# Performance work log

Hardware: AMD Instinct MI355X
Metric: run time of the kernel (lower is better)

Reference implementation:

```python
import jax, jax.numpy as jnp
import numpy as np

B, S, D, H = 256, 512, 128, 256  # batch, seq_len, input_dim, hidden_dim


def setup_inputs() -> dict:
    key = jax.random.key(0)
    ks = jax.random.split(key, 7)
    scale = 1.0 / np.sqrt(H)
    return {
        "x": jax.random.normal(ks[0], (B, S, D), dtype=jnp.float32),
        # WU_e: Linear(2H + S -> S, bias=False)
        "W_ue": jax.random.uniform(ks[1], (S, 2 * H + S), dtype=jnp.float32, minval=-scale, maxval=scale),
        # v_e: Linear(S -> 1, bias=False)
        "v_e": jax.random.uniform(ks[2], (1, S), dtype=jnp.float32, minval=-scale, maxval=scale),
        # LSTM params (PyTorch layout: gates order i,f,g,o)
        "W_ih": jax.random.uniform(ks[3], (4 * H, D), dtype=jnp.float32, minval=-scale, maxval=scale),
        "W_hh": jax.random.uniform(ks[4], (4 * H, H), dtype=jnp.float32, minval=-scale, maxval=scale),
        "b_ih": jax.random.uniform(ks[5], (4 * H,), dtype=jnp.float32, minval=-scale, maxval=scale),
        "b_hh": jax.random.uniform(ks[6], (4 * H,), dtype=jnp.float32, minval=-scale, maxval=scale),
    }


def reference(x, W_ue, v_e, W_ih, W_hh, b_ih, b_hh):
    b = x.shape[0]
    hdim = W_hh.shape[1]
    # Split WU_e into the part acting on (h,c) and the part acting on x rows.
    W_h = W_ue[:, : 2 * hdim]          # [S, 2H]
    W_x = W_ue[:, 2 * hdim:]           # [S, S]
    xT = jnp.transpose(x, (0, 2, 1))   # [B, D, S]
    # x contribution to attention logits is the same every step -> precompute.
    proj_x = jnp.einsum("bds,os->bdo", xT, W_x)  # [B, D, S]
    v = v_e[0]                          # [S]
    xs = jnp.transpose(x, (1, 0, 2))    # [S, B, D]

    def step(carry, x_t):
        h, c = carry                                    # [B, H] each
        hs = jnp.concatenate([h, c], axis=-1)           # [B, 2H]
        proj_h = hs @ W_h.T                             # [B, S]
        t = jnp.tanh(proj_h[:, None, :] + proj_x)       # [B, D, S]
        E = jnp.einsum("bds,s->bd", t, v)               # [B, D]
        alpha = jax.nn.softmax(E, axis=1)               # [B, D]
        inp = x_t * alpha                               # [B, D]
        gates = inp @ W_ih.T + b_ih + h @ W_hh.T + b_hh # [B, 4H]
        i, f, g, o = jnp.split(gates, 4, axis=-1)
        i = jax.nn.sigmoid(i)
        f = jax.nn.sigmoid(f)
        g = jnp.tanh(g)
        o = jax.nn.sigmoid(o)
        c_new = f * c + i * g
        h_new = o * jnp.tanh(c_new)
        return (h_new, c_new), h_new

    h0 = jnp.zeros((b, hdim), dtype=x.dtype)
    c0 = jnp.zeros((b, hdim), dtype=x.dtype)
    _, x_encoded = jax.lax.scan(step, (h0, c0), xs)  # [S, B, H]
    return x_encoded
```

## Files before the change

### kernel.cpp

```cpp
#include <hip/hip_runtime.h>
#include <hip/hip_bf16.h>

typedef __attribute__((ext_vector_type(8))) short bf16x8;
typedef __attribute__((ext_vector_type(4))) float f32x4;

#define C2LE 2.8853900817779268f
#define LOG2E 1.4426950408889634f
#define AGENT __HIP_MEMORY_SCOPE_AGENT
#define RLX __ATOMIC_RELAXED

static __device__ __forceinline__ float blo(unsigned q) { return __uint_as_float(q << 16); }
static __device__ __forceinline__ float bhi(unsigned q) { return __uint_as_float(q & 0xFFFF0000u); }
static __device__ __forceinline__ float rterm(float arg) {
  return __builtin_amdgcn_rcpf(1.0f + __builtin_amdgcn_exp2f(arg));
}
static __device__ __forceinline__ float sigm(float x) {
  return __builtin_amdgcn_rcpf(1.0f + __builtin_amdgcn_exp2f(-x * LOG2E));
}
static __device__ __forceinline__ float tanhe(float x) {
  return fmaf(-2.0f, __builtin_amdgcn_rcpf(1.0f + __builtin_amdgcn_exp2f(x * C2LE)), 1.0f);
}
static __device__ __forceinline__ unsigned packhilo(float x) {
  __hip_bfloat16 h = __float2bfloat16(x);
  float r = x - __bfloat162float(h);
  __hip_bfloat16 l = __float2bfloat16(r);
  return (unsigned)__bfloat16_as_ushort(h) | ((unsigned)__bfloat16_as_ushort(l) << 16);
}
static __device__ __forceinline__ void mkfrags(uint4 q0, uint4 q1, bf16x8& hi, bf16x8& lo) {
  uint4 h, l;
  h.x = __builtin_amdgcn_perm(q0.y, q0.x, 0x05040100u);
  h.y = __builtin_amdgcn_perm(q0.w, q0.z, 0x05040100u);
  h.z = __builtin_amdgcn_perm(q1.y, q1.x, 0x05040100u);
  h.w = __builtin_amdgcn_perm(q1.w, q1.z, 0x05040100u);
  l.x = __builtin_amdgcn_perm(q0.y, q0.x, 0x07060302u);
  l.y = __builtin_amdgcn_perm(q0.w, q0.z, 0x07060302u);
  l.z = __builtin_amdgcn_perm(q1.y, q1.x, 0x07060302u);
  l.w = __builtin_amdgcn_perm(q1.w, q1.z, 0x07060302u);
  hi = *(bf16x8*)&h;
  lo = *(bf16x8*)&l;
}

__global__ void k_pack_whB(const float* __restrict__ wue, __hip_bfloat16* __restrict__ wp) {
  for (int idx = blockIdx.x * blockDim.x + threadIdx.x; idx < 262144;
       idx += gridDim.x * blockDim.x) {
    int j = idx & 7, l = (idx >> 3) & 63, kap = (idx >> 9) & 15, nb = (idx >> 13) & 3,
        sl = idx >> 15;
    int o = sl * 64 + nb * 16 + (l & 15);
    int dim = kap * 32 + (l >> 4) * 8 + j;
    wp[idx] = __float2bfloat16(wue[o * 1024 + dim]);
  }
}
__global__ void k_pack_w3B(const float* __restrict__ wih, const float* __restrict__ whh,
                           __hip_bfloat16* __restrict__ wp) {
  for (int idx = blockIdx.x * blockDim.x + threadIdx.x; idx < 393216;
       idx += gridDim.x * blockDim.x) {
    int j = idx & 7, l = (idx >> 3) & 63;
    int ks = (idx >> 9) % 12, r = (idx >> 9) / 12;
    int nb = r & 7, sl = r >> 3;
    int n = nb * 16 + (l & 15);
    int g = (n >> 5) * 256 + sl * 32 + (n & 31);
    int k = ks * 32 + (l >> 4) * 8 + j;
    float v = (k < 128) ? wih[g * 128 + k] : whh[g * 256 + (k - 128)];
    wp[idx] = __float2bfloat16(v);
  }
}
__global__ void k_bsum(const float* __restrict__ bih, const float* __restrict__ bhh,
                       float* __restrict__ bs) {
  int idx = blockIdx.x * blockDim.x + threadIdx.x;
  if (idx < 1024) bs[idx] = bih[idx] + bhh[idx];
}
__global__ void k_wxt(const float* __restrict__ wue, float* __restrict__ wxt) {
  for (int idx = blockIdx.x * blockDim.x + threadIdx.x; idx < 512 * 512;
       idx += gridDim.x * blockDim.x) {
    int o = idx & 511, s = idx >> 9;
    wxt[idx] = wue[o * 1024 + 512 + s];
  }
}

__global__ __launch_bounds__(512) void k_projx(const float* __restrict__ x,
                                               const float* __restrict__ wxt,
                                               __hip_bfloat16* __restrict__ px2) {
  __shared__ alignas(16) float xsT[32][512];
  const int b = blockIdx.x;
  const int tid = threadIdx.x;
  for (int dt = 0; dt < 4; ++dt) {
    __syncthreads();
    const float4* xr = (const float4*)(x + ((size_t)b << 16) + (size_t)tid * 128 + dt * 32);
#pragma unroll
    for (int q = 0; q < 8; ++q) {
      float4 vx = xr[q];
      xsT[q * 4 + 0][tid] = vx.x;
      xsT[q * 4 + 1][tid] = vx.y;
      xsT[q * 4 + 2][tid] = vx.z;
      xsT[q * 4 + 3][tid] = vx.w;
    }
    __syncthreads();
    const int o = tid;
    float acc[32];
#pragma unroll
    for (int dd = 0; dd < 32; ++dd) acc[dd] = 0.f;
    for (int s4 = 0; s4 < 128; ++s4) {
      float w0 = wxt[(s4 * 4 + 0) * 512 + o];
      float w1 = wxt[(s4 * 4 + 1) * 512 + o];
      float w2 = wxt[(s4 * 4 + 2) * 512 + o];
      float w3 = wxt[(s4 * 4 + 3) * 512 + o];
#pragma unroll
      for (int dd = 0; dd < 32; ++dd) {
        float4 xv = *(const float4*)&xsT[dd][s4 * 4];
        acc[dd] = fmaf(w0, xv.x, fmaf(w1, xv.y, fmaf(w2, xv.z, fmaf(w3, xv.w, acc[dd]))));
      }
    }
    for (int dd = 0; dd < 32; ++dd) {
      px2[((size_t)b * 128 + dt * 32 + dd) * 512 + o] = __float2bfloat16(acc[dd] * C2LE);
    }
  }
}

static __device__ __forceinline__ void gbar(unsigned* ctr, unsigned target) {
  __syncthreads();
  if (threadIdx.x == 0) {
    __hip_atomic_fetch_add(ctr, 1u, RLX, AGENT);
    while (__hip_atomic_load(ctr, RLX, AGENT) < target) __builtin_amdgcn_s_sleep(1);
  }
  __syncthreads();
}

__global__ __launch_bounds__(1024) void k_main(
    const __hip_bfloat16* __restrict__ px2, const __hip_bfloat16* __restrict__ whB,
    const __hip_bfloat16* __restrict__ w3B, const float* __restrict__ bsum,
    const float* __restrict__ x, const float* __restrict__ ve,
    unsigned* __restrict__ hG, float* __restrict__ Eg, unsigned* __restrict__ ctrs,
    float* __restrict__ out) {
  __shared__ alignas(16) __hip_bfloat16 w3_l[49152];
  __shared__ alignas(16) unsigned hA[8192];
  __shared__ alignas(16) unsigned uA[2048];
  __shared__ float PHp[4][8][64];
  __shared__ float PH[512];
  __shared__ float gp[2][128][8];
  __shared__ float c_l[32][8];
  __shared__ float v_l[64];
  __shared__ float bs_l[128];
  __shared__ float zpart[16];
  __shared__ float vss_sh;

  const int grp = blockIdx.x & 31;
  const int sl = blockIdx.x >> 5;
  const int tid = threadIdx.x;
  const int lane = tid & 63;
  const int w = tid >> 6;
  const int b = tid >> 7;
  const int d = tid & 127;
  const int bG = grp * 8 + b;

  {
    const uint4* src = (const uint4*)(w3B + (size_t)sl * 49152);
    uint4* dst = (uint4*)w3_l;
    for (int i = tid; i < 6144; i += 1024) dst[i] = src[i];
  }
  bf16x8 whr[4];
  {
    const bf16x8* src =
        (const bf16x8*)whB + ((size_t)(sl * 4 + (w & 3)) * 16 + (w >> 2) * 4) * 64 + lane;
#pragma unroll
    for (int i = 0; i < 4; ++i) whr[i] = src[i * 64];
  }
  uint4 pxr[8];
  {
    const uint4* p4 = (const uint4*)(px2 + ((size_t)bG * 128 + d) * 512 + sl * 64);
#pragma unroll
    for (int i = 0; i < 8; ++i) pxr[i] = p4[i];
  }
  if (tid < 64) v_l[tid] = ve[sl * 64 + tid];
  if (tid < 128) bs_l[tid] = bsum[(tid >> 5) * 256 + sl * 32 + (tid & 31)];
  if (tid < 256) c_l[tid >> 3][tid & 7] = 0.f;
  for (int i = tid; i < 8192; i += 1024) hA[i] = 0;
  for (int i = tid; i < 2048; i += 1024) uA[i] = 0;
  if (tid == 0) {
    float s = 0.f;
    for (int i = 0; i < 64; ++i) s += ve[sl * 64 + i];
    vss_sh = s;
  }
  __syncthreads();
  const float vss = vss_sh;
  unsigned* ctrA = ctrs + grp * 64;
  unsigned* ctrB = ctrA + 32;

  for (int t = 0; t < 512; ++t) {
    const int par = t & 1;

    {
      const unsigned long long* hp =
          (const unsigned long long*)(hG + (size_t)(par * 32 + grp) * 4096) + tid * 2;
      unsigned long long a0 = __hip_atomic_load(hp, RLX, AGENT);
      unsigned long long a1 = __hip_atomic_load(hp + 1, RLX, AGENT);
      int p = tid * 4;
      int jb = p & 7, bb = (p >> 3) & 7, rest = p >> 6;
      uint4 q;
      q.x = (unsigned)a0;
      q.y = (unsigned)(a0 >> 32);
      q.z = (unsigned)a1;
      q.w = (unsigned)(a1 >> 32);
      *(uint4*)&hA[rest * 128 + bb * 8 + jb] = q;
    }
    if (tid < 128)
      __hip_atomic_store(Eg + (size_t)((1 - par) * 32 + grp) * 1024 + sl * 128 + tid, 0.f, RLX,
                         AGENT);
    __syncthreads();

    {
      const int kq = w >> 2, nb = w & 3;
      f32x4 acc = {0.f, 0.f, 0.f, 0.f};
#pragma unroll
      for (int i = 0; i < 4; ++i) {
        const uint4* ap = (const uint4*)&hA[((kq * 4 + i) * 64 + lane) * 8];
        uint4 q0 = ap[0], q1 = ap[1];
        bf16x8 ahi, alo;
        mkfrags(q0, q1, ahi, alo);
        acc = __builtin_amdgcn_mfma_f32_16x16x32_bf16(ahi, whr[i], acc, 0, 0, 0);
        acc = __builtin_amdgcn_mfma_f32_16x16x32_bf16(alo, whr[i], acc, 0, 0, 0);
      }
      if (lane < 32) {
        int r16 = lane >> 4, c16 = lane & 15;
#pragma unroll
        for (int rr = 0; rr < 4; ++rr) PHp[kq][r16 * 4 + rr][nb * 16 + c16] = acc[rr];
      }
    }
    __syncthreads();
    if (tid < 512)
      PH[tid] = (PHp[0][tid >> 6][tid & 63] + PHp[1][tid >> 6][tid & 63] +
                 PHp[2][tid >> 6][tid & 63] + PHp[3][tid >> 6][tid & 63]) *
                C2LE;
    __syncthreads();

    float xv = x[((size_t)bG * 512 + t) * 128 + d];
    {
      float R = 0.f;
      const float* PHb = &PH[b * 64];
#pragma unroll 2
      for (int s8 = 0; s8 < 8; ++s8) {
        uint4 q = pxr[s8];
        float4 pa = *(const float4*)&PHb[s8 * 8];
        float4 pb = *(const float4*)&PHb[s8 * 8 + 4];
        float4 va = *(const float4*)&v_l[s8 * 8];
        float4 vb = *(const float4*)&v_l[s8 * 8 + 4];
        R = fmaf(va.x, rterm(pa.x + blo(q.x)), R);
        R = fmaf(va.y, rterm(pa.y + bhi(q.x)), R);
        R = fmaf(va.z, rterm(pa.z + blo(q.y)), R);
        R = fmaf(va.w, rterm(pa.w + bhi(q.y)), R);
        R = fmaf(vb.x, rterm(pb.x + blo(q.z)), R);
        R = fmaf(vb.y, rterm(pb.y + bhi(q.z)), R);
        R = fmaf(vb.z, rterm(pb.z + blo(q.w)), R);
        R = fmaf(vb.w, rterm(pb.w + bhi(q.w)), R);
      }
      __hip_atomic_fetch_add(Eg + (size_t)(par * 32 + grp) * 1024 + b * 128 + d,
                             fmaf(-2.f, R, vss), RLX, AGENT);
    }
    gbar(ctrA, 8u * (t + 1));

    float Ev = __hip_atomic_load(Eg + (size_t)(par * 32 + grp) * 1024 + b * 128 + d, RLX, AGENT);
    float e = __builtin_amdgcn_exp2f(Ev * LOG2E);
    {
      float z = e;
#pragma unroll
      for (int m = 1; m < 64; m <<= 1) z += __shfl_xor(z, m);
      if (lane == 0) zpart[w] = z;
    }
    __syncthreads();
    {
      float zf = zpart[2 * b] + zpart[2 * b + 1];
      float u = xv * e * __builtin_amdgcn_rcpf(zf);
      uA[((d >> 5) * 64 + ((d >> 3) & 3) * 16 + b) * 8 + (d & 7)] = packhilo(u);
    }
    __syncthreads();

    {
      const int nb = w & 7, kh = w >> 3;
      f32x4 acc = {0.f, 0.f, 0.f, 0.f};
      const bf16x8* bp = (const bf16x8*)w3_l + ((size_t)nb * 12 + kh * 6) * 64 + lane;
#pragma unroll
      for (int i = 0; i < 6; ++i) {
        int ks = kh * 6 + i;
        const uint4* ap = (ks < 4) ? (const uint4*)&uA[(ks * 64 + lane) * 8]
                                   : (const uint4*)&hA[((ks - 4) * 64 + lane) * 8];
        uint4 q0 = ap[0], q1 = ap[1];
        bf16x8 ahi, alo;
        mkfrags(q0, q1, ahi, alo);
        bf16x8 bf = bp[i * 64];
        acc = __builtin_amdgcn_mfma_f32_16x16x32_bf16(ahi, bf, acc, 0, 0, 0);
        acc = __builtin_amdgcn_mfma_f32_16x16x32_bf16(alo, bf, acc, 0, 0, 0);
      }
      if (lane < 32) {
        int r16 = lane >> 4, c16 = lane & 15;
#pragma unroll
        for (int rr = 0; rr < 4; ++rr) gp[kh][nb * 16 + c16][r16 * 4 + rr] = acc[rr];
      }
    }
    __syncthreads();

    if (tid < 256) {
      int bb = tid & 7, jj = tid >> 3;
      float gi = gp[0][jj][bb] + gp[1][jj][bb] + bs_l[jj];
      float gf = gp[0][32 + jj][bb] + gp[1][32 + jj][bb] + bs_l[32 + jj];
      float gg = gp[0][64 + jj][bb] + gp[1][64 + jj][bb] + bs_l[64 + jj];
      float go = gp[0][96 + jj][bb] + gp[1][96 + jj][bb] + bs_l[96 + jj];
      float i_ = sigm(gi), f_ = sigm(gf), g_ = tanhe(gg), o_ = sigm(go);
      float c_new = fmaf(f_, c_l[jj][bb], i_ * g_);
      float h_new = o_ * tanhe(c_new);
      c_l[jj][bb] = c_new;
      __builtin_nontemporal_store(h_new,
                                  out + ((size_t)t * 256 + grp * 8 + bb) * 256 + sl * 32 + jj);
      int dd = sl * 32 + jj;
      int p = (((dd >> 5) * 4 + ((dd >> 3) & 3)) * 8 + bb) * 8 + (dd & 7);
      unsigned* hw = hG + (size_t)((1 - par) * 32 + grp) * 4096;
      __hip_atomic_store(hw + p, packhilo(h_new), RLX, AGENT);
      __hip_atomic_store(hw + p + 2048, packhilo(c_new), RLX, AGENT);
    }
    gbar(ctrB, 8u * (t + 1));
  }
}

extern "C" void kernel_launch(void* const* d_in, const int* in_sizes, int n_in,
                              void* d_out, int out_size, void* d_ws, size_t ws_size,
                              hipStream_t stream) {
  const float* x = (const float*)d_in[0];
  const float* wue = (const float*)d_in[1];
  const float* ve = (const float*)d_in[2];
  const float* wih = (const float*)d_in[3];
  const float* whh = (const float*)d_in[4];
  const float* bih = (const float*)d_in[5];
  const float* bhh = (const float*)d_in[6];
  float* out = (float*)d_out;

  char* ws = (char*)d_ws;
  __hip_bfloat16* px2 = (__hip_bfloat16*)(ws);
  __hip_bfloat16* whB = (__hip_bfloat16*)(ws + 33554432);
  __hip_bfloat16* w3B = (__hip_bfloat16*)(ws + 34078720);
  float* bsum = (float*)(ws + 34865152);
  float* Eg = (float*)(ws + 34869248);
  unsigned* ctrs = (unsigned*)(ws + 35131392);
  unsigned* hG = (unsigned*)(ws + 35139584);
  float* wxt = (float*)(ws + 36188160);

  k_pack_whB<<<1024, 256, 0, stream>>>(wue, whB);
  k_pack_w3B<<<1024, 256, 0, stream>>>(wih, whh, w3B);
  k_bsum<<<4, 256, 0, stream>>>(bih, bhh, bsum);
  k_wxt<<<256, 256, 0, stream>>>(wue, wxt);
  k_projx<<<256, 512, 0, stream>>>(x, wxt, px2);
  hipMemsetAsync(hG, 0, 1048576, stream);
  hipMemsetAsync(Eg, 0, 262144, stream);
  hipMemsetAsync(ctrs, 0, 8192, stream);
  k_main<<<256, 1024, 0, stream>>>(px2, whB, w3B, bsum, x, ve, hG, Eg, ctrs, out);
}
```

Before: 5.127 ms.

## Overlap hidden-state gate MFMA with barrier wait and swizzle LDS operand buffers

Moves the h/c half of the gate GEMM ahead of the first cross-block barrier so it runs while other blocks finish their attention partial sums. After the barrier only the small attention-input part of the GEMM remains. The h and u LDS operand buffers are split into two uint4 arrays with an XOR swizzle, and the gate partials get padding, both to reduce bank conflicts. The output store and the prefetch of the next x value now happen between the arrive and the wait of the second barrier. The cost is more live registers across the barrier and more complex indexing.

```diff
diff --git a/kernel.cpp b/kernel.cpp
--- a/kernel.cpp
+++ b/kernel.cpp
@@ -39,6 +39,7 @@
   hi = *(bf16x8*)&h;
   lo = *(bf16x8*)&l;
 }
+static __device__ __forceinline__ int swz(int e) { return e ^ ((e >> 4) & 7); }
 
 __global__ void k_pack_whB(const float* __restrict__ wue, __hip_bfloat16* __restrict__ wp) {
   for (int idx = blockIdx.x * blockDim.x + threadIdx.x; idx < 262144;
@@ -116,15 +117,6 @@
   }
 }
 
-static __device__ __forceinline__ void gbar(unsigned* ctr, unsigned target) {
-  __syncthreads();
-  if (threadIdx.x == 0) {
-    __hip_atomic_fetch_add(ctr, 1u, RLX, AGENT);
-    while (__hip_atomic_load(ctr, RLX, AGENT) < target) __builtin_amdgcn_s_sleep(1);
-  }
-  __syncthreads();
-}
-
 __global__ __launch_bounds__(1024) void k_main(
     const __hip_bfloat16* __restrict__ px2, const __hip_bfloat16* __restrict__ whB,
     const __hip_bfloat16* __restrict__ w3B, const float* __restrict__ bsum,
@@ -132,11 +124,13 @@
     unsigned* __restrict__ hG, float* __restrict__ Eg, unsigned* __restrict__ ctrs,
     float* __restrict__ out) {
   __shared__ alignas(16) __hip_bfloat16 w3_l[49152];
-  __shared__ alignas(16) unsigned hA[8192];
-  __shared__ alignas(16) unsigned uA[2048];
+  __shared__ alignas(16) uint4 hA0[1024];
+  __shared__ alignas(16) uint4 hA1[1024];
+  __shared__ alignas(16) uint4 uA0[256];
+  __shared__ alignas(16) uint4 uA1[256];
   __shared__ float PHp[4][8][64];
   __shared__ float PH[512];
-  __shared__ float gp[2][128][8];
+  __shared__ float gp[2][128][9];
   __shared__ float c_l[32][8];
   __shared__ float v_l[64];
   __shared__ float bs_l[128];
@@ -173,8 +167,15 @@
   if (tid < 64) v_l[tid] = ve[sl * 64 + tid];
   if (tid < 128) bs_l[tid] = bsum[(tid >> 5) * 256 + sl * 32 + (tid & 31)];
   if (tid < 256) c_l[tid >> 3][tid & 7] = 0.f;
-  for (int i = tid; i < 8192; i += 1024) hA[i] = 0;
-  for (int i = tid; i < 2048; i += 1024) uA[i] = 0;
+  {
+    uint4 z = {0, 0, 0, 0};
+    hA0[tid] = z;
+    hA1[tid] = z;
+    if (tid < 256) {
+      uA0[tid] = z;
+      uA1[tid] = z;
+    }
+  }
   if (tid == 0) {
     float s = 0.f;
     for (int i = 0; i < 64; ++i) s += ve[sl * 64 + i];
@@ -184,6 +185,7 @@
   const float vss = vss_sh;
   unsigned* ctrA = ctrs + grp * 64;
   unsigned* ctrB = ctrA + 32;
+  float xv = x[((size_t)bG * 512) * 128 + d];
 
   for (int t = 0; t < 512; ++t) {
     const int par = t & 1;
@@ -194,13 +196,15 @@
       unsigned long long a0 = __hip_atomic_load(hp, RLX, AGENT);
       unsigned long long a1 = __hip_atomic_load(hp + 1, RLX, AGENT);
       int p = tid * 4;
-      int jb = p & 7, bb = (p >> 3) & 7, rest = p >> 6;
+      int e = ((p >> 6) << 4) + ((p >> 3) & 7);
+      int ep = swz(e);
       uint4 q;
       q.x = (unsigned)a0;
       q.y = (unsigned)(a0 >> 32);
       q.z = (unsigned)a1;
       q.w = (unsigned)(a1 >> 32);
-      *(uint4*)&hA[rest * 128 + bb * 8 + jb] = q;
+      if (p & 4) hA1[ep] = q;
+      else hA0[ep] = q;
     }
     if (tid < 128)
       __hip_atomic_store(Eg + (size_t)((1 - par) * 32 + grp) * 1024 + sl * 128 + tid, 0.f, RLX,
@@ -212,8 +216,8 @@
       f32x4 acc = {0.f, 0.f, 0.f, 0.f};
 #pragma unroll
       for (int i = 0; i < 4; ++i) {
-        const uint4* ap = (const uint4*)&hA[((kq * 4 + i) * 64 + lane) * 8];
-        uint4 q0 = ap[0], q1 = ap[1];
+        int ep = swz((kq * 4 + i) * 64 + lane);
+        uint4 q0 = hA0[ep], q1 = hA1[ep];
         bf16x8 ahi, alo;
         mkfrags(q0, q1, ahi, alo);
         acc = __builtin_amdgcn_mfma_f32_16x16x32_bf16(ahi, whr[i], acc, 0, 0, 0);
@@ -232,7 +236,6 @@
                 C2LE;
     __syncthreads();
 
-    float xv = x[((size_t)bG * 512 + t) * 128 + d];
     {
       float R = 0.f;
       const float* PHb = &PH[b * 64];
@@ -255,7 +258,26 @@
       __hip_atomic_fetch_add(Eg + (size_t)(par * 32 + grp) * 1024 + b * 128 + d,
                              fmaf(-2.f, R, vss), RLX, AGENT);
     }
-    gbar(ctrA, 8u * (t + 1));
+
+    const int nb3 = w & 7, kh3 = w >> 3;
+    f32x4 acc3 = {0.f, 0.f, 0.f, 0.f};
+#pragma unroll
+    for (int i = 0; i < 4; ++i) {
+      int ks = 4 + kh3 * 4 + i;
+      int ep = swz((ks - 4) * 64 + lane);
+      uint4 q0 = hA0[ep], q1 = hA1[ep];
+      bf16x8 ahi, alo;
+      mkfrags(q0, q1, ahi, alo);
+      bf16x8 bf = ((const bf16x8*)w3_l)[((size_t)nb3 * 12 + ks) * 64 + lane];
+      acc3 = __builtin_amdgcn_mfma_f32_16x16x32_bf16(ahi, bf, acc3, 0, 0, 0);
+      acc3 = __builtin_amdgcn_mfma_f32_16x16x32_bf16(alo, bf, acc3, 0, 0, 0);
+    }
+    __syncthreads();
+    if (tid == 0) {
+      __hip_atomic_fetch_add(ctrA, 1u, RLX, AGENT);
+      while (__hip_atomic_load(ctrA, RLX, AGENT) < 8u * (t + 1)) __builtin_amdgcn_s_sleep(1);
+    }
+    __syncthreads();
 
     float Ev = __hip_atomic_load(Eg + (size_t)(par * 32 + grp) * 1024 + b * 128 + d, RLX, AGENT);
     float e = __builtin_amdgcn_exp2f(Ev * LOG2E);
@@ -269,34 +291,31 @@
     {
       float zf = zpart[2 * b] + zpart[2 * b + 1];
       float u = xv * e * __builtin_amdgcn_rcpf(zf);
-      uA[((d >> 5) * 64 + ((d >> 3) & 3) * 16 + b) * 8 + (d & 7)] = packhilo(u);
-    }
-    __syncthreads();
-
-    {
-      const int nb = w & 7, kh = w >> 3;
-      f32x4 acc = {0.f, 0.f, 0.f, 0.f};
-      const bf16x8* bp = (const bf16x8*)w3_l + ((size_t)nb * 12 + kh * 6) * 64 + lane;
-#pragma unroll
-      for (int i = 0; i < 6; ++i) {
-        int ks = kh * 6 + i;
-        const uint4* ap = (ks < 4) ? (const uint4*)&uA[(ks * 64 + lane) * 8]
-                                   : (const uint4*)&hA[((ks - 4) * 64 + lane) * 8];
-        uint4 q0 = ap[0], q1 = ap[1];
-        bf16x8 ahi, alo;
-        mkfrags(q0, q1, ahi, alo);
-        bf16x8 bf = bp[i * 64];
-        acc = __builtin_amdgcn_mfma_f32_16x16x32_bf16(ahi, bf, acc, 0, 0, 0);
-        acc = __builtin_amdgcn_mfma_f32_16x16x32_bf16(alo, bf, acc, 0, 0, 0);
-      }
-      if (lane < 32) {
-        int r16 = lane >> 4, c16 = lane & 15;
-#pragma unroll
-        for (int rr = 0; rr < 4; ++rr) gp[kh][nb * 16 + c16][r16 * 4 + rr] = acc[rr];
-      }
-    }
-    __syncthreads();
-
+      int ep = swz((d >> 5) * 64 + ((d >> 3) & 3) * 16 + b);
+      unsigned* dst = (d & 4) ? (unsigned*)&uA1[ep] : (unsigned*)&uA0[ep];
+      dst[d & 3] = packhilo(u);
+    }
+    __syncthreads();
+
+#pragma unroll
+    for (int i = 0; i < 2; ++i) {
+      int ks = kh3 * 2 + i;
+      int ep = swz(ks * 64 + lane);
+      uint4 q0 = uA0[ep], q1 = uA1[ep];
+      bf16x8 ahi, alo;
+      mkfrags(q0, q1, ahi, alo);
+      bf16x8 bf = ((const bf16x8*)w3_l)[((size_t)nb3 * 12 + ks) * 64 + lane];
+      acc3 = __builtin_amdgcn_mfma_f32_16x16x32_bf16(ahi, bf, acc3, 0, 0, 0);
+      acc3 = __builtin_amdgcn_mfma_f32_16x16x32_bf16(alo, bf, acc3, 0, 0, 0);
+    }
+    if (lane < 32) {
+      int r16 = lane >> 4, c16 = lane & 15;
+#pragma unroll
+      for (int rr = 0; rr < 4; ++rr) gp[kh3][nb3 * 16 + c16][r16 * 4 + rr] = acc3[rr];
+    }
+    __syncthreads();
+
+    float h_new;
     if (tid < 256) {
       int bb = tid & 7, jj = tid >> 3;
       float gi = gp[0][jj][bb] + gp[1][jj][bb] + bs_l[jj];
@@ -305,17 +324,28 @@
       float go = gp[0][96 + jj][bb] + gp[1][96 + jj][bb] + bs_l[96 + jj];
       float i_ = sigm(gi), f_ = sigm(gf), g_ = tanhe(gg), o_ = sigm(go);
       float c_new = fmaf(f_, c_l[jj][bb], i_ * g_);
-      float h_new = o_ * tanhe(c_new);
+      h_new = o_ * tanhe(c_new);
       c_l[jj][bb] = c_new;
-      __builtin_nontemporal_store(h_new,
-                                  out + ((size_t)t * 256 + grp * 8 + bb) * 256 + sl * 32 + jj);
       int dd = sl * 32 + jj;
       int p = (((dd >> 5) * 4 + ((dd >> 3) & 3)) * 8 + bb) * 8 + (dd & 7);
       unsigned* hw = hG + (size_t)((1 - par) * 32 + grp) * 4096;
       __hip_atomic_store(hw + p, packhilo(h_new), RLX, AGENT);
       __hip_atomic_store(hw + p + 2048, packhilo(c_new), RLX, AGENT);
     }
-    gbar(ctrB, 8u * (t + 1));
+    __syncthreads();
+    if (tid == 0) __hip_atomic_fetch_add(ctrB, 1u, RLX, AGENT);
+    if (tid < 256) {
+      int bb = tid & 7, jj = tid >> 3;
+      __builtin_nontemporal_store(h_new,
+                                  out + ((size_t)t * 256 + grp * 8 + bb) * 256 + sl * 32 + jj);
+    }
+    int tn = (t < 511) ? t + 1 : 511;
+    float xv_n = x[((size_t)bG * 512 + tn) * 128 + d];
+    if (tid == 0) {
+      while (__hip_atomic_load(ctrB, RLX, AGENT) < 8u * (t + 1)) __builtin_amdgcn_s_sleep(1);
+    }
+    __syncthreads();
+    xv = xv_n;
   }
 }
 
```

After: 4.916 ms. -4.1%, faster.
